# Performance work log

Measured on AMD Instinct MI355X. Metric: run time of the kernel, lower is better.

The kernel has to match this reference:

```python
import jax, jax.numpy as jnp
import numpy as np

N_NODES = 50000
N_EDGES = 640000
IN_DIM = 128
HID = 128
OUT_DIM = 16
BATCH = 2
EPS = 1e-5


def setup_inputs() -> dict:
    key = jax.random.key(0)
    ks = jax.random.split(key, 12)
    x = jax.random.normal(ks[0], (BATCH, N_NODES, IN_DIM), dtype=jnp.float32)
    edge_index = jax.random.randint(ks[1], (2, N_EDGES), 0, N_NODES, dtype=jnp.int32)
    # learned per-edge log-weights (initialized ~0 like nn.Parameter(zeros), small noise for a nontrivial test)
    edge_weight_param = 0.01 * jax.random.normal(ks[2], (N_EDGES,), dtype=jnp.float32)
    s1 = 1.0 / np.sqrt(IN_DIM)
    s2 = 1.0 / np.sqrt(HID)
    W1 = jax.random.uniform(ks[3], (IN_DIM, HID), minval=-s1, maxval=s1, dtype=jnp.float32)
    b1 = jnp.zeros((HID,), jnp.float32)
    W2 = jax.random.uniform(ks[4], (HID, HID), minval=-s2, maxval=s2, dtype=jnp.float32)
    b2 = jnp.zeros((HID,), jnp.float32)
    g1 = jnp.ones((HID,), jnp.float32); be1 = jnp.zeros((HID,), jnp.float32)
    g2 = jnp.ones((HID,), jnp.float32); be2 = jnp.zeros((HID,), jnp.float32)
    Wc = jax.random.uniform(ks[5], (HID, OUT_DIM), minval=-s2, maxval=s2, dtype=jnp.float32)
    bc = jax.random.uniform(ks[6], (OUT_DIM,), minval=-s2, maxval=s2, dtype=jnp.float32)
    return {"x": x, "edge_index": edge_index, "edge_weight_param": edge_weight_param,
            "W1": W1, "b1": b1, "W2": W2, "b2": b2,
            "g1": g1, "be1": be1, "g2": g2, "be2": be2,
            "Wc": Wc, "bc": bc}


def _gcn_norm(edge_index, edge_weight):
    # PyG GCNConv: add self-loops (weight 1), symmetric D^-1/2 A D^-1/2 normalization
    row = jnp.concatenate([edge_index[0], jnp.arange(N_NODES, dtype=edge_index.dtype)])
    col = jnp.concatenate([edge_index[1], jnp.arange(N_NODES, dtype=edge_index.dtype)])
    ew = jnp.concatenate([edge_weight, jnp.ones((N_NODES,), edge_weight.dtype)])
    deg = jax.ops.segment_sum(ew, col, num_segments=N_NODES)
    dinv = jnp.where(deg > 0, jax.lax.rsqrt(jnp.maximum(deg, 1e-30)), 0.0)
    norm = dinv[row] * ew * dinv[col]
    return row, col, norm


def _gcn_conv(x, W, b, row, col, norm):
    # x: [B, N, F_in] -> [B, N, F_out]; gather-scale-scatter over edges
    xw = x @ W                                   # [B, N, H]
    msg = xw[:, row, :] * norm[None, :, None]    # [B, E+N, H]
    out = jax.vmap(lambda m: jax.ops.segment_sum(m, col, num_segments=N_NODES))(msg)
    return out + b


def _batchnorm(h, gamma, beta):
    # training-mode BN over flattened (B*N) rows, biased variance, eps=1e-5
    B, N, F = h.shape
    hf = h.reshape(-1, F)
    mu = hf.mean(axis=0)
    var = hf.var(axis=0)
    return (((hf - mu) * jax.lax.rsqrt(var + EPS)) * gamma + beta).reshape(B, N, F)


def reference(x, edge_index, edge_weight_param, W1, b1, W2, b2, g1, be1, g2, be2, Wc, bc):
    edge_weight = jnp.exp(edge_weight_param)  # learned exp edge weights
    row, col, norm = _gcn_norm(edge_index, edge_weight)
    h = jax.nn.relu(_gcn_conv(x, W1, b1, row, col, norm))
    h = _batchnorm(h, g1, be1)
    # dropout is identity in eval / deterministic reference
    h = jax.nn.relu(_gcn_conv(h, W2, b2, row, col, norm))
    h = _batchnorm(h, g2, be2)
    return h @ Wc + bc  # [B, N, OUT_DIM]
```

## Files before the change

### kernel.cpp

```cpp
#include <hip/hip_runtime.h>
#include <hip/hip_bf16.h>
#include <cstdint>
#include <cstddef>

#define N_NODES 50000
#define N_EDGES 640000
#define ROWS    100000
#define HID     128
#define OUTD    16
#define AGG_BLOCKS 2048
#define MID_BLOCKS 32
#define SCAN_BLOCKS 196
#define GEMM_BLOCKS 512
#define GEMM_TILES  (ROWS / 16)

typedef __attribute__((ext_vector_type(8))) uint16_t ushort8;
typedef __attribute__((ext_vector_type(8))) __bf16   bf16x8;
typedef __attribute__((ext_vector_type(4))) float    floatx4;

union FragU { ushort8 u; bf16x8 b; };

__device__ __forceinline__ float bf_lo(uint32_t u){
  union { uint32_t u; float f; } c; c.u = u << 16; return c.f;
}
__device__ __forceinline__ float bf_hi(uint32_t u){
  union { uint32_t u; float f; } c; c.u = u & 0xffff0000u; return c.f;
}
__device__ __forceinline__ uint16_t f2bf(float f){
  union { float f; uint32_t u; } c; c.f = f;
  uint32_t u = c.u;
  uint32_t r = (u + 0x7fffu + ((u >> 16) & 1u)) >> 16;
  return (uint16_t)r;
}

__global__ void k_init(unsigned long long* __restrict__ dc){
  int i = blockIdx.x * 256 + threadIdx.x;
  if (i < N_NODES) dc[i] = 0ull;
}

__global__ void k_edge1(const int* __restrict__ ei, const float* __restrict__ ewp,
                        unsigned long long* __restrict__ dc, unsigned int* __restrict__ slot){
  int e = blockIdx.x * 256 + threadIdx.x;
  if (e < N_EDGES){
    float w = expf(ewp[e]);
    int c = ei[N_EDGES + e];
    unsigned long long inc = (1ull << 44) | (unsigned long long)(w * 1048576.0f + 0.5f);
    unsigned long long old = atomicAdd(&dc[c], inc);
    slot[e] = (unsigned int)(old >> 44);
  }
}

__global__ void k_scan_bsum(const unsigned long long* __restrict__ dc, int* __restrict__ bsum,
                            float* __restrict__ dinv){
  __shared__ int sd[256];
  int tid = threadIdx.x;
  int i = blockIdx.x * 256 + tid;
  int cnt = 0;
  if (i < N_NODES){
    unsigned long long v = dc[i];
    cnt = (int)(v >> 44);
    float deg = 1.0f + (float)((double)(v & ((1ull << 44) - 1)) * (1.0 / 1048576.0));
    dinv[i] = 1.0f / sqrtf(deg);
  }
  sd[tid] = cnt;
  __syncthreads();
  for (int off = 128; off > 0; off >>= 1){
    if (tid < off) sd[tid] += sd[tid + off];
    __syncthreads();
  }
  if (tid == 0) bsum[blockIdx.x] = sd[0];
}

__global__ void k_scan_excl(int* __restrict__ bsum){
  __shared__ int sd[256];
  int tid = threadIdx.x;
  sd[tid] = (tid < SCAN_BLOCKS) ? bsum[tid] : 0;
  __syncthreads();
  if (tid == 0){
    int run = 0;
    for (int i = 0; i < SCAN_BLOCKS; i++){ int t = sd[i]; sd[i] = run; run += t; }
  }
  __syncthreads();
  if (tid < SCAN_BLOCKS) bsum[tid] = sd[tid];
}

__global__ void k_scan_write(const unsigned long long* __restrict__ dc, const int* __restrict__ bsum,
                             int* __restrict__ rp){
  __shared__ int sd[256];
  int tid = threadIdx.x;
  int i = blockIdx.x * 256 + tid;
  int v = (i < N_NODES) ? (int)(dc[i] >> 44) : 0;
  sd[tid] = v;
  __syncthreads();
  for (int off = 1; off < 256; off <<= 1){
    int t = (tid >= off) ? sd[tid - off] : 0;
    __syncthreads();
    sd[tid] += t;
    __syncthreads();
  }
  if (i < N_NODES) rp[i] = bsum[blockIdx.x] + sd[tid] - v;
  if (blockIdx.x == 0 && tid == 0) rp[N_NODES] = N_EDGES;
}

__global__ void k_fill(const int* __restrict__ ei, const float* __restrict__ ewp,
                       const float* __restrict__ dinv, const unsigned int* __restrict__ slot,
                       const int* __restrict__ rp, unsigned long long* __restrict__ edg){
  int e = blockIdx.x * 256 + threadIdx.x;
  if (e < N_EDGES){
    int r = ei[e];
    int c = ei[N_EDGES + e];
    float w = expf(ewp[e]);
    float nrm = dinv[r] * w * dinv[c];
    int p = rp[c] + (int)slot[e];
    edg[p] = ((unsigned long long)__float_as_uint(nrm) << 32) | (unsigned int)r;
  }
}

__global__ void k_wpack(const float* __restrict__ W, const float* __restrict__ sca,
                        uint16_t* __restrict__ WP){
  int t = blockIdx.x * 256 + threadIdx.x;
  int L = t & 63;
  int s = (t >> 6) & 3;
  int c = t >> 8;
  int n = (c >> 1) * 32 + 2 * (L & 15) + (c & 1);
  int k0 = s * 32 + (L >> 4) * 8;
  ushort8 r;
#pragma unroll
  for (int j = 0; j < 8; j++){
    float w = W[(size_t)(k0 + j) * HID + n];
    if (sca) w *= sca[k0 + j];
    r[j] = f2bf(w);
  }
  *((ushort8*)(WP + (size_t)t * 8)) = r;
}

__global__ void k_wpackc(const float* __restrict__ Wc, const float* __restrict__ sca,
                         uint16_t* __restrict__ WPC){
  int t = threadIdx.x;
  int L = t & 63;
  int s = t >> 6;
  int n = L & 15;
  int k0 = s * 32 + (L >> 4) * 8;
  ushort8 r;
#pragma unroll
  for (int j = 0; j < 8; j++)
    r[j] = f2bf(sca[k0 + j] * Wc[(size_t)(k0 + j) * OUTD + n]);
  *((ushort8*)(WPC + (size_t)t * 8)) = r;
}

__global__ void k_cvec(const float* __restrict__ shf, const float* __restrict__ W,
                       const float* __restrict__ bias, float* __restrict__ cv, int ncol, int stride){
  int j = threadIdx.x;
  if (j < ncol){
    float a = bias ? bias[j] : 0.f;
    for (int k = 0; k < HID; k++) a = fmaf(shf[k], W[(size_t)k * stride + j], a);
    cv[j] = a;
  }
}

template <bool FP32_IN>
__global__ __launch_bounds__(256, 2) void k_gemm_mfma(const void* __restrict__ Xv,
                                                      const uint16_t* __restrict__ WP,
                                                      uint16_t* __restrict__ Y){
  const int lane = threadIdx.x & 63;
  const int wid  = threadIdx.x >> 6;
  const int gw   = blockIdx.x * 4 + wid;
  const int nw   = GEMM_BLOCKS * 4;
  const int m    = lane & 15;
  const int kq   = lane >> 4;

  FragU wf[8][4];
#pragma unroll
  for (int c = 0; c < 8; c++)
#pragma unroll
    for (int s = 0; s < 4; s++)
      wf[c][s].u = *((const ushort8*)(WP + (size_t)(((c * 4 + s) * 64 + lane) * 8)));

  uint32_t* Yu = (uint32_t*)Y;
  for (int t = gw; t < GEMM_TILES; t += nw){
    const int row0 = t * 16;
    FragU af[4];
    if (FP32_IN){
      const float* X = (const float*)Xv;
#pragma unroll
      for (int s = 0; s < 4; s++){
        const float* p = X + (size_t)(row0 + m) * HID + s * 32 + kq * 8;
        floatx4 f0 = *((const floatx4*)p);
        floatx4 f1 = *((const floatx4*)(p + 4));
        ushort8 r;
#pragma unroll
        for (int j = 0; j < 4; j++){ r[j] = f2bf(f0[j]); r[j + 4] = f2bf(f1[j]); }
        af[s].u = r;
      }
    } else {
      const uint16_t* X = (const uint16_t*)Xv;
#pragma unroll
      for (int s = 0; s < 4; s++)
        af[s].u = *((const ushort8*)(X + (size_t)(row0 + m) * HID + s * 32 + kq * 8));
    }

    floatx4 acc[8];
#pragma unroll
    for (int c = 0; c < 8; c++) acc[c] = floatx4{0.f, 0.f, 0.f, 0.f};
#pragma unroll
    for (int s = 0; s < 4; s++)
#pragma unroll
      for (int c = 0; c < 8; c++)
        acc[c] = __builtin_amdgcn_mfma_f32_16x16x32_bf16(af[s].b, wf[c][s].b, acc[c], 0, 0, 0);

#pragma unroll
    for (int t4 = 0; t4 < 4; t4++)
#pragma unroll
      for (int i = 0; i < 4; i++){
        uint32_t pr = (uint32_t)f2bf(acc[2 * t4][i]) | ((uint32_t)f2bf(acc[2 * t4 + 1][i]) << 16);
        Yu[(size_t)(row0 + kq * 4 + i) * 64 + t4 * 16 + m] = pr;
      }
  }
}

__global__ __launch_bounds__(256) void k_cls_mfma(const uint16_t* __restrict__ H,
                                                  const uint16_t* __restrict__ WPC,
                                                  const float* __restrict__ cvec,
                                                  float* __restrict__ out){
  const int lane = threadIdx.x & 63;
  const int wid  = threadIdx.x >> 6;
  const int gw   = blockIdx.x * 4 + wid;
  const int nw   = GEMM_BLOCKS * 4;
  const int m    = lane & 15;
  const int kq   = lane >> 4;

  FragU wf[4];
#pragma unroll
  for (int s = 0; s < 4; s++)
    wf[s].u = *((const ushort8*)(WPC + (size_t)((s * 64 + lane) * 8)));
  const float cv = cvec[m];

  for (int t = gw; t < GEMM_TILES; t += nw){
    const int row0 = t * 16;
    FragU af[4];
#pragma unroll
    for (int s = 0; s < 4; s++)
      af[s].u = *((const ushort8*)(H + (size_t)(row0 + m) * HID + s * 32 + kq * 8));
    floatx4 acc = floatx4{0.f, 0.f, 0.f, 0.f};
#pragma unroll
    for (int s = 0; s < 4; s++)
      acc = __builtin_amdgcn_mfma_f32_16x16x32_bf16(af[s].b, wf[s].b, acc, 0, 0, 0);
#pragma unroll
    for (int i = 0; i < 4; i++)
      out[(size_t)(row0 + kq * 4 + i) * OUTD + m] = acc[i] + cv;
  }
}

__global__ __launch_bounds__(256) void k_agg(const uint16_t* __restrict__ XW,
                                             const int* __restrict__ rp,
                                             const unsigned long long* __restrict__ edg,
                                             const float* __restrict__ dinv,
                                             const float* __restrict__ bias,
                                             const float* __restrict__ cvec,
                                             uint16_t* __restrict__ H,
                                             float* __restrict__ psum,
                                             float* __restrict__ pssq){
  __shared__ float lsum[128];
  __shared__ float lssq[128];
  const int tid = threadIdx.x;
  if (tid < 128){ lsum[tid] = 0.f; lssq[tid] = 0.f; }
  __syncthreads();

  const int lane = tid & 63;
  const int wid  = tid >> 6;
  const int gw   = blockIdx.x * 4 + wid;
  const int nw   = AGG_BLOCKS * 4;
  const uint32_t* Xu = (const uint32_t*)XW;
  uint32_t* Hu = (uint32_t*)H;
  const int f0 = lane * 2;
  const float b0 = bias[f0], b1 = bias[f0 + 1];
  const float c0 = cvec ? cvec[f0] : 0.f;
  const float c1 = cvec ? cvec[f0 + 1] : 0.f;
  float ts0 = 0.f, ts1 = 0.f, tq0 = 0.f, tq1 = 0.f;

  int node = gw;
  if (node < N_NODES){
    int e0 = rp[node], e1 = rp[node + 1];
    float di = dinv[node];
    uint32_t s0 = Xu[(size_t)node * 64 + lane];
    uint32_t s1 = Xu[(size_t)(N_NODES + node) * 64 + lane];
    while (true){
      const int nn = node + nw;
      const bool more = (nn < N_NODES);
      int ne0 = 0, ne1 = 0; float ndi = 0.f; uint32_t ns0 = 0, ns1 = 0;
      if (more){
        ne0 = rp[nn]; ne1 = rp[nn + 1];
        ndi = dinv[nn];
        ns0 = Xu[(size_t)nn * 64 + lane];
        ns1 = Xu[(size_t)(N_NODES + nn) * 64 + lane];
      }

      const float sn = di * di;
      float a0x = sn * bf_lo(s0), a0y = sn * bf_hi(s0);
      float a1x = sn * bf_lo(s1), a1y = sn * bf_hi(s1);
      float wsum = sn;
      int e = e0;
      for (; e + 8 <= e1; e += 8){
        unsigned long long rec[8];
#pragma unroll
        for (int u = 0; u < 8; u++) rec[u] = edg[e + u];
        uint32_t q0[8], q1[8];
#pragma unroll
        for (int u = 0; u < 8; u++){
          size_t src = (uint32_t)rec[u];
          q0[u] = Xu[src * 64 + lane];
          q1[u] = Xu[(N_NODES + src) * 64 + lane];
        }
#pragma unroll
        for (int u = 0; u < 8; u++){
          float w = __uint_as_float((uint32_t)(rec[u] >> 32));
          a0x = fmaf(w, bf_lo(q0[u]), a0x); a0y = fmaf(w, bf_hi(q0[u]), a0y);
          a1x = fmaf(w, bf_lo(q1[u]), a1x); a1y = fmaf(w, bf_hi(q1[u]), a1y);
          wsum += w;
        }
      }
      for (; e + 4 <= e1; e += 4){
        unsigned long long rec[4];
#pragma unroll
        for (int u = 0; u < 4; u++) rec[u] = edg[e + u];
        uint32_t q0[4], q1[4];
#pragma unroll
        for (int u = 0; u < 4; u++){
          size_t src = (uint32_t)rec[u];
          q0[u] = Xu[src * 64 + lane];
          q1[u] = Xu[(N_NODES + src) * 64 + lane];
        }
#pragma unroll
        for (int u = 0; u < 4; u++){
          float w = __uint_as_float((uint32_t)(rec[u] >> 32));
          a0x = fmaf(w, bf_lo(q0[u]), a0x); a0y = fmaf(w, bf_hi(q0[u]), a0y);
          a1x = fmaf(w, bf_lo(q1[u]), a1x); a1y = fmaf(w, bf_hi(q1[u]), a1y);
          wsum += w;
        }
      }
      for (; e + 2 <= e1; e += 2){
        unsigned long long ra = edg[e], rb = edg[e + 1];
        size_t sa = (uint32_t)ra, sb = (uint32_t)rb;
        uint32_t qa0 = Xu[sa * 64 + lane], qa1 = Xu[(N_NODES + sa) * 64 + lane];
        uint32_t qb0 = Xu[sb * 64 + lane], qb1 = Xu[(N_NODES + sb) * 64 + lane];
        float wa = __uint_as_float((uint32_t)(ra >> 32));
        float wb = __uint_as_float((uint32_t)(rb >> 32));
        a0x = fmaf(wa, bf_lo(qa0), a0x); a0y = fmaf(wa, bf_hi(qa0), a0y);
        a1x = fmaf(wa, bf_lo(qa1), a1x); a1y = fmaf(wa, bf_hi(qa1), a1y);
        a0x = fmaf(wb, bf_lo(qb0), a0x); a0y = fmaf(wb, bf_hi(qb0), a0y);
        a1x = fmaf(wb, bf_lo(qb1), a1x); a1y = fmaf(wb, bf_hi(qb1), a1y);
        wsum += wa + wb;
      }
      for (; e < e1; e++){
        unsigned long long rec = edg[e];
        size_t src = (uint32_t)rec;
        float w = __uint_as_float((uint32_t)(rec >> 32));
        uint32_t g0 = Xu[src * 64 + lane];
        uint32_t g1 = Xu[(N_NODES + src) * 64 + lane];
        a0x = fmaf(w, bf_lo(g0), a0x); a0y = fmaf(w, bf_hi(g0), a0y);
        a1x = fmaf(w, bf_lo(g1), a1x); a1y = fmaf(w, bf_hi(g1), a1y);
        wsum += w;
      }
      a0x = fmaxf(fmaf(wsum, c0, a0x) + b0, 0.f); a0y = fmaxf(fmaf(wsum, c1, a0y) + b1, 0.f);
      a1x = fmaxf(fmaf(wsum, c0, a1x) + b0, 0.f); a1y = fmaxf(fmaf(wsum, c1, a1y) + b1, 0.f);
      Hu[(size_t)node * 64 + lane]             = (uint32_t)f2bf(a0x) | ((uint32_t)f2bf(a0y) << 16);
      Hu[(size_t)(N_NODES + node) * 64 + lane] = (uint32_t)f2bf(a1x) | ((uint32_t)f2bf(a1y) << 16);
      ts0 += a0x + a1x; ts1 += a0y + a1y;
      tq0 += a0x * a0x + a1x * a1x; tq1 += a0y * a0y + a1y * a1y;

      if (!more) break;
      node = nn; e0 = ne0; e1 = ne1; di = ndi; s0 = ns0; s1 = ns1;
    }
  }

  atomicAdd(&lsum[f0],     ts0); atomicAdd(&lsum[f0 + 1], ts1);
  atomicAdd(&lssq[f0],     tq0); atomicAdd(&lssq[f0 + 1], tq1);
  __syncthreads();
  if (tid < 128){
    psum[(size_t)blockIdx.x * 128 + tid] = lsum[tid];
    pssq[(size_t)blockIdx.x * 128 + tid] = lssq[tid];
  }
}

__global__ __launch_bounds__(256) void k_bnmid(const float* __restrict__ psum,
                                               const float* __restrict__ pssq,
                                               float* __restrict__ msum,
                                               float* __restrict__ mssq){
  __shared__ float ss[2][128];
  __shared__ float sq[2][128];
  const int tid = threadIdx.x;
  const int f  = tid & 127;
  const int sl = tid >> 7;
  const int rows_per = AGG_BLOCKS / MID_BLOCKS;
  const int base = blockIdx.x * rows_per;
  float s = 0.f, q = 0.f;
  for (int r = base + sl; r < base + rows_per; r += 2){
    s += psum[(size_t)r * 128 + f];
    q += pssq[(size_t)r * 128 + f];
  }
  ss[sl][f] = s; sq[sl][f] = q;
  __syncthreads();
  if (tid < 128){
    msum[(size_t)blockIdx.x * 128 + tid] = ss[0][tid] + ss[1][tid];
    mssq[(size_t)blockIdx.x * 128 + tid] = sq[0][tid] + sq[1][tid];
  }
}

__global__ __launch_bounds__(128) void k_bnfin(const float* __restrict__ msum,
                                               const float* __restrict__ mssq,
                                               const float* __restrict__ gamma,
                                               const float* __restrict__ beta,
                                               float* __restrict__ sca,
                                               float* __restrict__ shf){
  const int f = threadIdx.x;
  float S = 0.f, Q = 0.f;
#pragma unroll
  for (int b = 0; b < MID_BLOCKS; b++){
    S += msum[(size_t)b * 128 + f];
    Q += mssq[(size_t)b * 128 + f];
  }
  const float inv = 1.0f / (float)ROWS;
  float mu = S * inv;
  float var = fmaxf(Q * inv - mu * mu, 0.f);
  float rstd = 1.0f / sqrtf(var + 1e-5f);
  float sc = gamma[f] * rstd;
  sca[f] = sc;
  shf[f] = fmaf(-mu, sc, beta[f]);
}

extern "C" void kernel_launch(void* const* d_in, const int* in_sizes, int n_in,
                              void* d_out, int out_size, void* d_ws, size_t ws_size,
                              hipStream_t stream){
  const float* x   = (const float*)d_in[0];
  const int*   ei  = (const int*)d_in[1];
  const float* ewp = (const float*)d_in[2];
  const float* W1  = (const float*)d_in[3];
  const float* b1  = (const float*)d_in[4];
  const float* W2  = (const float*)d_in[5];
  const float* b2  = (const float*)d_in[6];
  const float* g1  = (const float*)d_in[7];
  const float* be1 = (const float*)d_in[8];
  const float* g2  = (const float*)d_in[9];
  const float* be2 = (const float*)d_in[10];
  const float* Wc  = (const float*)d_in[11];
  const float* bc  = (const float*)d_in[12];
  float* out = (float*)d_out;

  char* wsb = (char*)d_ws;
  size_t off = 0;
  auto give = [&](size_t bytes) -> void* {
    void* p = wsb + off;
    off = (off + bytes + 255) & ~(size_t)255;
    return p;
  };
  uint16_t* XW  = (uint16_t*)give((size_t)ROWS * 128 * 2);
  uint16_t* Hb  = (uint16_t*)give((size_t)ROWS * 128 * 2);
  unsigned long long* DC  = (unsigned long long*)give((size_t)N_NODES * 8);
  unsigned long long* EDG = (unsigned long long*)give((size_t)N_EDGES * 8);
  unsigned int* SLOT = (unsigned int*)give((size_t)N_EDGES * 4);
  float* DINV   = (float*)give((size_t)N_NODES * 4);
  int*   RP     = (int*)give((size_t)(N_NODES + 1) * 4);
  int*   BSUM   = (int*)give(1024);
  float* PSUM   = (float*)give((size_t)AGG_BLOCKS * 128 * 4);
  float* PSSQ   = (float*)give((size_t)AGG_BLOCKS * 128 * 4);
  float* MSUM   = (float*)give((size_t)MID_BLOCKS * 128 * 4);
  float* MSSQ   = (float*)give((size_t)MID_BLOCKS * 128 * 4);
  float* SCA1   = (float*)give(512);
  float* SHF1   = (float*)give(512);
  float* SCA2   = (float*)give(512);
  float* SHF2   = (float*)give(512);
  uint16_t* WP1 = (uint16_t*)give((size_t)HID * HID * 2);
  uint16_t* WP2 = (uint16_t*)give((size_t)HID * HID * 2);
  uint16_t* WPC = (uint16_t*)give((size_t)HID * OUTD * 2);
  float* C2     = (float*)give(512);
  float* CVC    = (float*)give(64);
  (void)ws_size; (void)n_in; (void)in_sizes; (void)out_size;

  const int nb_nodes = (N_NODES + 255) / 256;
  const int nb_edges = (N_EDGES + 255) / 256;

  k_init<<<nb_nodes, 256, 0, stream>>>(DC);
  k_edge1<<<nb_edges, 256, 0, stream>>>(ei, ewp, DC, SLOT);
  k_scan_bsum<<<SCAN_BLOCKS, 256, 0, stream>>>(DC, BSUM, DINV);
  k_scan_excl<<<1, 256, 0, stream>>>(BSUM);
  k_scan_write<<<SCAN_BLOCKS, 256, 0, stream>>>(DC, BSUM, RP);
  k_fill<<<nb_edges, 256, 0, stream>>>(ei, ewp, DINV, SLOT, RP, EDG);
  k_wpack<<<8, 256, 0, stream>>>(W1, nullptr, WP1);

  k_gemm_mfma<true><<<GEMM_BLOCKS, 256, 0, stream>>>(x, WP1, XW);
  k_agg<<<AGG_BLOCKS, 256, 0, stream>>>(XW, RP, EDG, DINV, b1, nullptr, Hb, PSUM, PSSQ);
  k_bnmid<<<MID_BLOCKS, 256, 0, stream>>>(PSUM, PSSQ, MSUM, MSSQ);
  k_bnfin<<<1, 128, 0, stream>>>(MSUM, MSSQ, g1, be1, SCA1, SHF1);

  k_wpack<<<8, 256, 0, stream>>>(W2, SCA1, WP2);
  k_cvec<<<1, 128, 0, stream>>>(SHF1, W2, nullptr, C2, HID, HID);
  k_gemm_mfma<false><<<GEMM_BLOCKS, 256, 0, stream>>>(Hb, WP2, XW);
  k_agg<<<AGG_BLOCKS, 256, 0, stream>>>(XW, RP, EDG, DINV, b2, C2, Hb, PSUM, PSSQ);
  k_bnmid<<<MID_BLOCKS, 256, 0, stream>>>(PSUM, PSSQ, MSUM, MSSQ);
  k_bnfin<<<1, 128, 0, stream>>>(MSUM, MSSQ, g2, be2, SCA2, SHF2);

  k_wpackc<<<1, 256, 0, stream>>>(Wc, SCA2, WPC);
  k_cvec<<<1, 128, 0, stream>>>(SHF2, Wc, bc, CVC, OUTD, OUTD);
  k_cls_mfma<<<GEMM_BLOCKS, 256, 0, stream>>>(Hb, WPC, CVC, out);
}
```

Before: 359.0 us.

## Fuse setup kernels and co-schedule edge-degree atomics with first GEMM

Merges the degree-buffer init with W1 packing, interleaves the edge-degree atomic blocks with the layer-1 MFMA GEMM blocks in one launch, folds the block-sum exclusive scan into the scan-write kernel, and combines BN finalize with weight packing and bias-vector computation for both later layers. This removes several small serial launches and lets the latency-bound atomic pass overlap the compute-bound GEMM. In exchange, each scan block redundantly reduces the prefix of block sums, and the BN finalize is recomputed in every prep block.

```diff
diff --git a/kernel.cpp b/kernel.cpp
--- a/kernel.cpp
+++ b/kernel.cpp
@@ -13,6 +13,8 @@
 #define SCAN_BLOCKS 196
 #define GEMM_BLOCKS 512
 #define GEMM_TILES  (ROWS / 16)
+#define EG_BLOCKS   3000
+#define EG_GEMM_WAVES 2000
 
 typedef __attribute__((ext_vector_type(8))) uint16_t ushort8;
 typedef __attribute__((ext_vector_type(8))) __bf16   bf16x8;
@@ -33,20 +35,96 @@
   return (uint16_t)r;
 }
 
-__global__ void k_init(unsigned long long* __restrict__ dc){
-  int i = blockIdx.x * 256 + threadIdx.x;
-  if (i < N_NODES) dc[i] = 0ull;
-}
-
-__global__ void k_edge1(const int* __restrict__ ei, const float* __restrict__ ewp,
-                        unsigned long long* __restrict__ dc, unsigned int* __restrict__ slot){
-  int e = blockIdx.x * 256 + threadIdx.x;
-  if (e < N_EDGES){
+__device__ __forceinline__ void pack_w(int t, const float* __restrict__ W,
+                                       const float* sca ,
+                                       uint16_t* __restrict__ WP){
+  int L = t & 63;
+  int s = (t >> 6) & 3;
+  int c = t >> 8;
+  int n = (c >> 1) * 32 + 2 * (L & 15) + (c & 1);
+  int k0 = s * 32 + (L >> 4) * 8;
+  ushort8 r;
+#pragma unroll
+  for (int j = 0; j < 8; j++){
+    float w = W[(size_t)(k0 + j) * HID + n];
+    if (sca) w *= sca[k0 + j];
+    r[j] = f2bf(w);
+  }
+  *((ushort8*)(WP + (size_t)t * 8)) = r;
+}
+
+__global__ void k_initpack(unsigned long long* __restrict__ dc,
+                           const float* __restrict__ W1, uint16_t* __restrict__ WP1){
+  int b = blockIdx.x;
+  if (b < SCAN_BLOCKS){
+    int i = b * 256 + threadIdx.x;
+    if (i < N_NODES) dc[i] = 0ull;
+  } else {
+    pack_w((b - SCAN_BLOCKS) * 256 + threadIdx.x, W1, nullptr, WP1);
+  }
+}
+
+__global__ __launch_bounds__(256, 2) void k_edge_gemm1(const int* __restrict__ ei,
+                                                       const float* __restrict__ ewp,
+                                                       unsigned long long* __restrict__ dc,
+                                                       unsigned int* __restrict__ slot,
+                                                       const float* __restrict__ X,
+                                                       const uint16_t* __restrict__ WP,
+                                                       uint16_t* __restrict__ Y){
+  const int b = blockIdx.x;
+  const int g = b % 6;
+  if (g != 0){
+    const int eb = (b / 6) * 5 + (g - 1);
+    const int e = eb * 256 + threadIdx.x;
     float w = expf(ewp[e]);
     int c = ei[N_EDGES + e];
     unsigned long long inc = (1ull << 44) | (unsigned long long)(w * 1048576.0f + 0.5f);
     unsigned long long old = atomicAdd(&dc[c], inc);
     slot[e] = (unsigned int)(old >> 44);
+    return;
+  }
+  const int lane = threadIdx.x & 63;
+  const int wid  = threadIdx.x >> 6;
+  const int gw   = (b / 6) * 4 + wid;
+  const int m    = lane & 15;
+  const int kq   = lane >> 4;
+
+  FragU wf[8][4];
+#pragma unroll
+  for (int c = 0; c < 8; c++)
+#pragma unroll
+    for (int s = 0; s < 4; s++)
+      wf[c][s].u = *((const ushort8*)(WP + (size_t)(((c * 4 + s) * 64 + lane) * 8)));
+
+  uint32_t* Yu = (uint32_t*)Y;
+  for (int t = gw; t < GEMM_TILES; t += EG_GEMM_WAVES){
+    const int row0 = t * 16;
+    FragU af[4];
+#pragma unroll
+    for (int s = 0; s < 4; s++){
+      const float* p = X + (size_t)(row0 + m) * HID + s * 32 + kq * 8;
+      floatx4 f0 = *((const floatx4*)p);
+      floatx4 f1 = *((const floatx4*)(p + 4));
+      ushort8 r;
+#pragma unroll
+      for (int j = 0; j < 4; j++){ r[j] = f2bf(f0[j]); r[j + 4] = f2bf(f1[j]); }
+      af[s].u = r;
+    }
+    floatx4 acc[8];
+#pragma unroll
+    for (int c = 0; c < 8; c++) acc[c] = floatx4{0.f, 0.f, 0.f, 0.f};
+#pragma unroll
+    for (int s = 0; s < 4; s++)
+#pragma unroll
+      for (int c = 0; c < 8; c++)
+        acc[c] = __builtin_amdgcn_mfma_f32_16x16x32_bf16(af[s].b, wf[c][s].b, acc[c], 0, 0, 0);
+#pragma unroll
+    for (int t4 = 0; t4 < 4; t4++)
+#pragma unroll
+      for (int i = 0; i < 4; i++){
+        uint32_t pr = (uint32_t)f2bf(acc[2 * t4][i]) | ((uint32_t)f2bf(acc[2 * t4 + 1][i]) << 16);
+        Yu[(size_t)(row0 + kq * 4 + i) * 64 + t4 * 16 + m] = pr;
+      }
   }
 }
 
@@ -71,23 +149,19 @@
   if (tid == 0) bsum[blockIdx.x] = sd[0];
 }
 
-__global__ void k_scan_excl(int* __restrict__ bsum){
+__global__ void k_scan_write(const unsigned long long* __restrict__ dc, const int* __restrict__ bsum,
+                             int* __restrict__ rp){
+  __shared__ int sb[256];
   __shared__ int sd[256];
   int tid = threadIdx.x;
-  sd[tid] = (tid < SCAN_BLOCKS) ? bsum[tid] : 0;
-  __syncthreads();
-  if (tid == 0){
-    int run = 0;
-    for (int i = 0; i < SCAN_BLOCKS; i++){ int t = sd[i]; sd[i] = run; run += t; }
-  }
-  __syncthreads();
-  if (tid < SCAN_BLOCKS) bsum[tid] = sd[tid];
-}
-
-__global__ void k_scan_write(const unsigned long long* __restrict__ dc, const int* __restrict__ bsum,
-                             int* __restrict__ rp){
-  __shared__ int sd[256];
-  int tid = threadIdx.x;
+  sb[tid] = (tid < SCAN_BLOCKS && tid < blockIdx.x) ? bsum[tid] : 0;
+  __syncthreads();
+  for (int off = 128; off > 0; off >>= 1){
+    if (tid < off) sb[tid] += sb[tid + off];
+    __syncthreads();
+  }
+  const int base = sb[0];
+
   int i = blockIdx.x * 256 + tid;
   int v = (i < N_NODES) ? (int)(dc[i] >> 44) : 0;
   sd[tid] = v;
@@ -98,7 +172,7 @@
     sd[tid] += t;
     __syncthreads();
   }
-  if (i < N_NODES) rp[i] = bsum[blockIdx.x] + sd[tid] - v;
+  if (i < N_NODES) rp[i] = base + sd[tid] - v;
   if (blockIdx.x == 0 && tid == 0) rp[N_NODES] = N_EDGES;
 }
 
@@ -116,52 +190,9 @@
   }
 }
 
-__global__ void k_wpack(const float* __restrict__ W, const float* __restrict__ sca,
-                        uint16_t* __restrict__ WP){
-  int t = blockIdx.x * 256 + threadIdx.x;
-  int L = t & 63;
-  int s = (t >> 6) & 3;
-  int c = t >> 8;
-  int n = (c >> 1) * 32 + 2 * (L & 15) + (c & 1);
-  int k0 = s * 32 + (L >> 4) * 8;
-  ushort8 r;
-#pragma unroll
-  for (int j = 0; j < 8; j++){
-    float w = W[(size_t)(k0 + j) * HID + n];
-    if (sca) w *= sca[k0 + j];
-    r[j] = f2bf(w);
-  }
-  *((ushort8*)(WP + (size_t)t * 8)) = r;
-}
-
-__global__ void k_wpackc(const float* __restrict__ Wc, const float* __restrict__ sca,
-                         uint16_t* __restrict__ WPC){
-  int t = threadIdx.x;
-  int L = t & 63;
-  int s = t >> 6;
-  int n = L & 15;
-  int k0 = s * 32 + (L >> 4) * 8;
-  ushort8 r;
-#pragma unroll
-  for (int j = 0; j < 8; j++)
-    r[j] = f2bf(sca[k0 + j] * Wc[(size_t)(k0 + j) * OUTD + n]);
-  *((ushort8*)(WPC + (size_t)t * 8)) = r;
-}
-
-__global__ void k_cvec(const float* __restrict__ shf, const float* __restrict__ W,
-                       const float* __restrict__ bias, float* __restrict__ cv, int ncol, int stride){
-  int j = threadIdx.x;
-  if (j < ncol){
-    float a = bias ? bias[j] : 0.f;
-    for (int k = 0; k < HID; k++) a = fmaf(shf[k], W[(size_t)k * stride + j], a);
-    cv[j] = a;
-  }
-}
-
-template <bool FP32_IN>
-__global__ __launch_bounds__(256, 2) void k_gemm_mfma(const void* __restrict__ Xv,
-                                                      const uint16_t* __restrict__ WP,
-                                                      uint16_t* __restrict__ Y){
+__global__ __launch_bounds__(256, 2) void k_gemm2(const uint16_t* __restrict__ X,
+                                                  const uint16_t* __restrict__ WP,
+                                                  uint16_t* __restrict__ Y){
   const int lane = threadIdx.x & 63;
   const int wid  = threadIdx.x >> 6;
   const int gw   = blockIdx.x * 4 + wid;
@@ -180,25 +211,9 @@
   for (int t = gw; t < GEMM_TILES; t += nw){
     const int row0 = t * 16;
     FragU af[4];
-    if (FP32_IN){
-      const float* X = (const float*)Xv;
-#pragma unroll
-      for (int s = 0; s < 4; s++){
-        const float* p = X + (size_t)(row0 + m) * HID + s * 32 + kq * 8;
-        floatx4 f0 = *((const floatx4*)p);
-        floatx4 f1 = *((const floatx4*)(p + 4));
-        ushort8 r;
-#pragma unroll
-        for (int j = 0; j < 4; j++){ r[j] = f2bf(f0[j]); r[j + 4] = f2bf(f1[j]); }
-        af[s].u = r;
-      }
-    } else {
-      const uint16_t* X = (const uint16_t*)Xv;
-#pragma unroll
-      for (int s = 0; s < 4; s++)
-        af[s].u = *((const ushort8*)(X + (size_t)(row0 + m) * HID + s * 32 + kq * 8));
-    }
-
+#pragma unroll
+    for (int s = 0; s < 4; s++)
+      af[s].u = *((const ushort8*)(X + (size_t)(row0 + m) * HID + s * 32 + kq * 8));
     floatx4 acc[8];
 #pragma unroll
     for (int c = 0; c < 8; c++) acc[c] = floatx4{0.f, 0.f, 0.f, 0.f};
@@ -207,7 +222,6 @@
 #pragma unroll
       for (int c = 0; c < 8; c++)
         acc[c] = __builtin_amdgcn_mfma_f32_16x16x32_bf16(af[s].b, wf[c][s].b, acc[c], 0, 0, 0);
-
 #pragma unroll
     for (int t4 = 0; t4 < 4; t4++)
 #pragma unroll
@@ -406,26 +420,71 @@
   }
 }
 
-__global__ __launch_bounds__(128) void k_bnfin(const float* __restrict__ msum,
-                                               const float* __restrict__ mssq,
-                                               const float* __restrict__ gamma,
-                                               const float* __restrict__ beta,
-                                               float* __restrict__ sca,
-                                               float* __restrict__ shf){
-  const int f = threadIdx.x;
-  float S = 0.f, Q = 0.f;
-#pragma unroll
-  for (int b = 0; b < MID_BLOCKS; b++){
-    S += msum[(size_t)b * 128 + f];
-    Q += mssq[(size_t)b * 128 + f];
-  }
-  const float inv = 1.0f / (float)ROWS;
-  float mu = S * inv;
-  float var = fmaxf(Q * inv - mu * mu, 0.f);
-  float rstd = 1.0f / sqrtf(var + 1e-5f);
-  float sc = gamma[f] * rstd;
-  sca[f] = sc;
-  shf[f] = fmaf(-mu, sc, beta[f]);
+__device__ __forceinline__ void bn_finalize_lds(const float* __restrict__ msum,
+                                                const float* __restrict__ mssq,
+                                                const float* __restrict__ gamma,
+                                                const float* __restrict__ beta,
+                                                float* ssc, float* ssh){
+  const int tid = threadIdx.x;
+  if (tid < 128){
+    float S = 0.f, Q = 0.f;
+#pragma unroll
+    for (int b = 0; b < MID_BLOCKS; b++){
+      S += msum[(size_t)b * 128 + tid];
+      Q += mssq[(size_t)b * 128 + tid];
+    }
+    const float inv = 1.0f / (float)ROWS;
+    float mu = S * inv;
+    float var = fmaxf(Q * inv - mu * mu, 0.f);
+    float rstd = 1.0f / sqrtf(var + 1e-5f);
+    float sc = gamma[tid] * rstd;
+    ssc[tid] = sc;
+    ssh[tid] = fmaf(-mu, sc, beta[tid]);
+  }
+  __syncthreads();
+}
+
+__global__ void k_prep2(const float* __restrict__ msum, const float* __restrict__ mssq,
+                        const float* __restrict__ gamma, const float* __restrict__ beta,
+                        const float* __restrict__ W2,
+                        uint16_t* __restrict__ WP2, float* __restrict__ C2){
+  __shared__ float ssc[128];
+  __shared__ float ssh[128];
+  bn_finalize_lds(msum, mssq, gamma, beta, ssc, ssh);
+  if (blockIdx.x < 8){
+    pack_w(blockIdx.x * 256 + threadIdx.x, W2, ssc, WP2);
+  } else if (threadIdx.x < 128){
+    const int j = threadIdx.x;
+    float a = 0.f;
+    for (int k = 0; k < HID; k++) a = fmaf(ssh[k], W2[(size_t)k * HID + j], a);
+    C2[j] = a;
+  }
+}
+
+__global__ void k_prepc(const float* __restrict__ msum, const float* __restrict__ mssq,
+                        const float* __restrict__ gamma, const float* __restrict__ beta,
+                        const float* __restrict__ Wc, const float* __restrict__ bc,
+                        uint16_t* __restrict__ WPC, float* __restrict__ CVC){
+  __shared__ float ssc[128];
+  __shared__ float ssh[128];
+  bn_finalize_lds(msum, mssq, gamma, beta, ssc, ssh);
+  if (blockIdx.x == 0){
+    int t = threadIdx.x;
+    int L = t & 63;
+    int s = t >> 6;
+    int n = L & 15;
+    int k0 = s * 32 + (L >> 4) * 8;
+    ushort8 r;
+#pragma unroll
+    for (int j = 0; j < 8; j++)
+      r[j] = f2bf(ssc[k0 + j] * Wc[(size_t)(k0 + j) * OUTD + n]);
+    *((ushort8*)(WPC + (size_t)t * 8)) = r;
+  } else if (threadIdx.x < OUTD){
+    const int j = threadIdx.x;
+    float a = bc[j];
+    for (int k = 0; k < HID; k++) a = fmaf(ssh[k], Wc[(size_t)k * OUTD + j], a);
+    CVC[j] = a;
+  }
 }
 
 extern "C" void kernel_launch(void* const* d_in, const int* in_sizes, int n_in,
@@ -465,10 +524,6 @@
   float* PSSQ   = (float*)give((size_t)AGG_BLOCKS * 128 * 4);
   float* MSUM   = (float*)give((size_t)MID_BLOCKS * 128 * 4);
   float* MSSQ   = (float*)give((size_t)MID_BLOCKS * 128 * 4);
-  float* SCA1   = (float*)give(512);
-  float* SHF1   = (float*)give(512);
-  float* SCA2   = (float*)give(512);
-  float* SHF2   = (float*)give(512);
   uint16_t* WP1 = (uint16_t*)give((size_t)HID * HID * 2);
   uint16_t* WP2 = (uint16_t*)give((size_t)HID * HID * 2);
   uint16_t* WPC = (uint16_t*)give((size_t)HID * OUTD * 2);
@@ -476,30 +531,17 @@
   float* CVC    = (float*)give(64);
   (void)ws_size; (void)n_in; (void)in_sizes; (void)out_size;
 
-  const int nb_nodes = (N_NODES + 255) / 256;
-  const int nb_edges = (N_EDGES + 255) / 256;
-
-  k_init<<<nb_nodes, 256, 0, stream>>>(DC);
-  k_edge1<<<nb_edges, 256, 0, stream>>>(ei, ewp, DC, SLOT);
+  k_initpack<<<SCAN_BLOCKS + 8, 256, 0, stream>>>(DC, W1, WP1);
+  k_edge_gemm1<<<EG_BLOCKS, 256, 0, stream>>>(ei, ewp, DC, SLOT, x, WP1, XW);
   k_scan_bsum<<<SCAN_BLOCKS, 256, 0, stream>>>(DC, BSUM, DINV);
-  k_scan_excl<<<1, 256, 0, stream>>>(BSUM);
   k_scan_write<<<SCAN_BLOCKS, 256, 0, stream>>>(DC, BSUM, RP);
-  k_fill<<<nb_edges, 256, 0, stream>>>(ei, ewp, DINV, SLOT, RP, EDG);
-  k_wpack<<<8, 256, 0, stream>>>(W1, nullptr, WP1);
-
-  k_gemm_mfma<true><<<GEMM_BLOCKS, 256, 0, stream>>>(x, WP1, XW);
+  k_fill<<<(N_EDGES + 255) / 256, 256, 0, stream>>>(ei, ewp, DINV, SLOT, RP, EDG);
   k_agg<<<AGG_BLOCKS, 256, 0, stream>>>(XW, RP, EDG, DINV, b1, nullptr, Hb, PSUM, PSSQ);
   k_bnmid<<<MID_BLOCKS, 256, 0, stream>>>(PSUM, PSSQ, MSUM, MSSQ);
-  k_bnfin<<<1, 128, 0, stream>>>(MSUM, MSSQ, g1, be1, SCA1, SHF1);
-
-  k_wpack<<<8, 256, 0, stream>>>(W2, SCA1, WP2);
-  k_cvec<<<1, 128, 0, stream>>>(SHF1, W2, nullptr, C2, HID, HID);
-  k_gemm_mfma<false><<<GEMM_BLOCKS, 256, 0, stream>>>(Hb, WP2, XW);
+  k_prep2<<<9, 256, 0, stream>>>(MSUM, MSSQ, g1, be1, W2, WP2, C2);
+  k_gemm2<<<GEMM_BLOCKS, 256, 0, stream>>>(Hb, WP2, XW);
   k_agg<<<AGG_BLOCKS, 256, 0, stream>>>(XW, RP, EDG, DINV, b2, C2, Hb, PSUM, PSSQ);
   k_bnmid<<<MID_BLOCKS, 256, 0, stream>>>(PSUM, PSSQ, MSUM, MSSQ);
-  k_bnfin<<<1, 128, 0, stream>>>(MSUM, MSSQ, g2, be2, SCA2, SHF2);
-
-  k_wpackc<<<1, 256, 0, stream>>>(Wc, SCA2, WPC);
-  k_cvec<<<1, 128, 0, stream>>>(SHF2, Wc, bc, CVC, OUTD, OUTD);
+  k_prepc<<<2, 256, 0, stream>>>(MSUM, MSSQ, g2, be2, Wc, bc, WPC, CVC);
   k_cls_mfma<<<GEMM_BLOCKS, 256, 0, stream>>>(Hb, WPC, CVC, out);
 }
```

Measured after the change: 334.8 us. -6.7%, faster.
